# Optimization experiments

Hardware: AMD Instinct MI355X
Metric: run time of the kernel (lower is better)

## Reference

```python
import jax, jax.numpy as jnp
import numpy as np

OUT = 7          # roi_align output size
SR = 2           # sampling_ratio
SCALE = 1.0 / 16.0
T_OUT = 16       # F.interpolate temporal target
EPS = 1e-6


def setup_inputs() -> dict:
    key = jax.random.key(0)
    ks = jax.random.split(key, 12)
    B, Cin, Cout, T, H, W = 1, 1536, 3072, 16, 14, 14
    y = jax.random.normal(ks[0], (B, Cin, T, H, W), jnp.float32)
    x_t = jax.random.normal(ks[1], (B, Cout, T, H, W), jnp.float32)
    # ROIs in 224x224 image coords (spatial_scale = 1/16): one [1,4] box per frame
    x1 = jax.random.uniform(ks[2], (T,), minval=0.0, maxval=112.0)
    y1 = jax.random.uniform(ks[3], (T,), minval=0.0, maxval=112.0)
    x2 = jnp.minimum(x1 + jax.random.uniform(ks[4], (T,), minval=80.0, maxval=112.0), 224.0)
    y2 = jnp.minimum(y1 + jax.random.uniform(ks[5], (T,), minval=80.0, maxval=112.0), 224.0)
    rois = jnp.stack([x1, y1, x2, y2], axis=-1)[:, None, :]  # [T,1,4]
    conv_w = jax.random.normal(ks[6], (Cout, Cin), jnp.float32) * 0.02
    conv_b = jax.random.normal(ks[7], (Cout,), jnp.float32) * 0.02
    gamma = 1.0 + 0.1 * jax.random.normal(ks[8], (Cout,), jnp.float32)
    beta = 0.1 * jax.random.normal(ks[9], (Cout,), jnp.float32)
    run_mean = 0.1 * jax.random.normal(ks[10], (Cout,), jnp.float32)
    run_var = jax.random.uniform(ks[11], (Cout,), minval=0.5, maxval=1.5)
    return dict(y=y, x_t=x_t, rois=rois, conv_w=conv_w, conv_b=conv_b,
                gamma=gamma, beta=beta, run_mean=run_mean, run_var=run_var)


def _bilinear_sample(img, ys, xs):
    # img: [C,H,W]; ys: [Sy]; xs: [Sx] -> [C,Sy,Sx]; torchvision roi_align semantics
    C, H, W = img.shape
    oy = (ys < -1.0) | (ys > H)
    ox = (xs < -1.0) | (xs > W)
    yc = jnp.clip(ys, 0.0, H - 1)
    xc = jnp.clip(xs, 0.0, W - 1)
    y0 = jnp.floor(yc).astype(jnp.int32)
    x0 = jnp.floor(xc).astype(jnp.int32)
    y1i = jnp.minimum(y0 + 1, H - 1)
    x1i = jnp.minimum(x0 + 1, W - 1)
    ly = yc - y0
    lx = xc - x0
    g = lambda yi, xi: img[:, yi[:, None], xi[None, :]]  # [C,Sy,Sx]
    wy0, wy1 = (1.0 - ly)[:, None], ly[:, None]
    wx0, wx1 = (1.0 - lx)[None, :], lx[None, :]
    val = (wy0 * wx0 * g(y0, x0) + wy0 * wx1 * g(y0, x1i)
           + wy1 * wx0 * g(y1i, x0) + wy1 * wx1 * g(y1i, x1i))
    mask = (~oy)[:, None] & (~ox)[None, :]
    return jnp.where(mask[None], val, 0.0)


def _roi_align(feat, boxes):
    # feat: [N,C,H,W]; boxes: [N,4] (one box per image, aligned=False, sampling_ratio=2)
    N, C, H, W = feat.shape
    b = boxes * SCALE
    bx1, by1, bx2, by2 = b[:, 0], b[:, 1], b[:, 2], b[:, 3]
    rw = jnp.maximum(bx2 - bx1, 1.0)
    rh = jnp.maximum(by2 - by1, 1.0)
    bw, bh = rw / OUT, rh / OUT
    # sample positions per bin: (bin + (i+0.5)/SR) * bin_size
    pos = (jnp.arange(OUT, dtype=jnp.float32)[:, None]
           + (jnp.arange(SR, dtype=jnp.float32)[None, :] + 0.5) / SR).reshape(-1)  # [OUT*SR]
    ys = by1[:, None] + pos[None, :] * bh[:, None]
    xs = bx1[:, None] + pos[None, :] * bw[:, None]
    vals = jax.vmap(_bilinear_sample)(feat, ys, xs)  # [N,C,OUT*SR,OUT*SR]
    return vals.reshape(N, C, OUT, SR, OUT, SR).mean(axis=(3, 5))


def reference(y, x_t, rois, conv_w, conv_b, gamma, beta, run_mean, run_var):
    B, Cout, T, Hf, Wf = x_t.shape
    # 1x1x1 Conv3d, stride (1,2,2)
    ys = y[:, :, :, ::2, ::2]                                   # [B,Cin,T,7,7]
    yp = jnp.einsum('bcthw,oc->bothw', ys, conv_w) + conv_b[None, :, None, None, None]
    # BatchNorm3d (eval, eps=1e-6) + GELU (exact)
    inv = gamma / jnp.sqrt(run_var + EPS)
    yp = (yp - run_mean[None, :, None, None, None]) * inv[None, :, None, None, None] \
         + beta[None, :, None, None, None]
    yp = jax.nn.gelu(yp, approximate=False)
    # nearest temporal interpolation to T_OUT (identity when Tin == 16)
    Tin = yp.shape[2]
    tidx = (jnp.arange(T_OUT) * Tin) // T_OUT
    yp = yp[:, :, tidx]                                          # [B,Cout,16,7,7]
    # fusion branch: roi_align over (B*T) frames
    ff = jnp.transpose(x_t, (0, 2, 1, 3, 4)).reshape(B * T, Cout, Hf, Wf)
    boxes = rois[:, 0, :]                                        # [T,4]
    mr = _roi_align(ff, boxes)                                   # [B*T,Cout,7,7]
    mr = jnp.transpose(mr.reshape(B, T, Cout, OUT, OUT), (0, 2, 1, 3, 4))
    weighted = yp * mr                                           # [B,Cout,16,7,7]
    # per-frame 7x7 scatter-write into zeros, same window logic as the torch loop
    bs = boxes * SCALE
    sxi = jnp.floor(bs[:, 0]).astype(jnp.int32)
    syi = jnp.floor(bs[:, 1]).astype(jnp.int32)
    exi = jnp.ceil(bs[:, 2]).astype(jnp.int32)
    eyi = jnp.ceil(bs[:, 3]).astype(jnp.int32)
    ml = jnp.where(sxi + 7 < 14, sxi, exi - 7)
    mt = jnp.where(syi + 7 < 14, syi, eyi - 7)
    def place(w_t, t_off, l_off):  # w_t: [B,Cout,7,7]
        z = jnp.zeros((B, Cout, Hf, Wf), w_t.dtype)
        return jax.lax.dynamic_update_slice(z, w_t, (0, 0, t_off, l_off))
    new_face = jax.vmap(place, in_axes=(2, 0, 0), out_axes=2)(weighted, mt, ml)
    return new_face + x_t
```

## Files before the change

kernel.cpp:

```cpp
#include <hip/hip_runtime.h>

#define KD 1536
#define ND 3072
#define MD 784
#define TT 16

typedef __attribute__((ext_vector_type(8))) short short8;
typedef __attribute__((ext_vector_type(4))) float floatx4;

__device__ __forceinline__ unsigned short f2bf(float f) {
    unsigned int x = __float_as_uint(f);
    unsigned int r = (x + 0x7fffu + ((x >> 16) & 1u)) >> 16;
    return (unsigned short)r;
}

__device__ __forceinline__ void gld_lds16(const unsigned short* g, unsigned short* l) {
    __builtin_amdgcn_global_load_lds((const __attribute__((address_space(1))) void*)g,
                                     (__attribute__((address_space(3))) void*)l, 16, 0, 0);
}

__global__ __launch_bounds__(256) void prep_k(const float* __restrict__ y,
                                              const float* __restrict__ conv_w,
                                              unsigned short* __restrict__ Ap,
                                              unsigned short* __restrict__ Bp) {
    __shared__ float sm[64 * 197];
    const int bid = blockIdx.x;
    const int tid = threadIdx.x;

    if (bid < 384) {
        const int t2 = bid / 24, kc = bid % 24;
        for (int i4 = tid; i4 < 64 * 49; i4 += 256) {
            int c = i4 / 49, p4 = i4 % 49;
            float4 v = *(const float4*)(y + (size_t)(kc * 64 + c) * 3136 + t2 * 196 + p4 * 4);
            float* d = &sm[c * 197 + p4 * 4];
            d[0] = v.x; d[1] = v.y; d[2] = v.z; d[3] = v.w;
        }
        __syncthreads();
        for (int item = tid; item < 64 * 49; item += 256) {
            int c = item & 63, ij = item >> 6;
            int i = ij / 7, j = ij % 7;
            Ap[(size_t)(t2 * 49 + ij) * KD + kc * 64 + c] =
                f2bf(sm[c * 197 + (2 * i) * 14 + 2 * j]);
        }
    } else {
        size_t base = (size_t)(bid - 384) * 12288;
#pragma unroll
        for (int v = 0; v < 12; ++v) {
            size_t e = base + v * 1024 + tid * 4;
            float4 w4 = *(const float4*)(conv_w + e);
            ushort4 o;
            o.x = f2bf(w4.x); o.y = f2bf(w4.y); o.z = f2bf(w4.z); o.w = f2bf(w4.w);
            *(ushort4*)(Bp + e) = o;
        }
    }
}

__global__ __launch_bounds__(256, 3) void gemm_k(const unsigned short* __restrict__ Ap,
                                                 const unsigned short* __restrict__ Bp,
                                                 const float* __restrict__ cb,
                                                 const float* __restrict__ gm,
                                                 const float* __restrict__ bt,
                                                 const float* __restrict__ rm,
                                                 const float* __restrict__ rv,
                                                 const float* __restrict__ x_t,
                                                 const float* __restrict__ rois,
                                                 float* __restrict__ out) {
    __shared__ float sm[64 * 197];
    __shared__ float wx0s[14], wx1s[14], wy0s[14], wy1s[14];
    __shared__ int x0s[14], x1s[14], y0s[14], y1s[14], vxs[14], vys[14];

    unsigned short* const smem = (unsigned short*)sm;
    unsigned short* const As0 = smem;
    unsigned short* const As1 = smem + 4096;
    unsigned short* const Bs0 = smem + 8192;
    unsigned short* const Bs1 = smem + 12288;

    const int tid = threadIdx.x;
    const int n0 = blockIdx.x * 64;
    const int t = blockIdx.y;
    const int aRow0 = t * 49;
    const int wv = tid >> 6;
    const int lane = tid & 63;
    const int wm = wv >> 1, wn = wv & 1;
    const int l15 = lane & 15, quad = lane >> 4;
    const int prow = lane >> 3, pch = lane & 7;
    const int L = pch ^ (prow & 7);

    if (tid < 14) {
        float b0 = rois[t * 4 + 0] * 0.0625f, b1 = rois[t * 4 + 1] * 0.0625f;
        float b2 = rois[t * 4 + 2] * 0.0625f, b3 = rois[t * 4 + 3] * 0.0625f;
        float rw = fmaxf(b2 - b0, 1.0f), rh = fmaxf(b3 - b1, 1.0f);
        float bw = rw * (1.0f / 7.0f), bh = rh * (1.0f / 7.0f);
        int p = tid;
        float pos = (float)(p >> 1) + 0.25f + 0.5f * (float)(p & 1);
        float xs = b0 + pos * bw;
        float ysv = b1 + pos * bh;
        vxs[p] = (xs >= -1.0f && xs <= 14.0f);
        vys[p] = (ysv >= -1.0f && ysv <= 14.0f);
        float xc = fminf(fmaxf(xs, 0.0f), 13.0f);
        float yc = fminf(fmaxf(ysv, 0.0f), 13.0f);
        int x0 = (int)floorf(xc), y0 = (int)floorf(yc);
        x0s[p] = x0; y0s[p] = y0;
        x1s[p] = min(x0 + 1, 13); y1s[p] = min(y0 + 1, 13);
        float lx = xc - (float)x0, ly = yc - (float)y0;
        wx0s[p] = 1.0f - lx; wx1s[p] = lx; wy0s[p] = 1.0f - ly; wy1s[p] = ly;
    }

    const unsigned short* gbase;
    unsigned short *lb0, *lb1;
    if (wv < 2) {
        gbase = Ap + (size_t)(aRow0 + wv * 32 + prow) * KD + L * 8;
        lb0 = &As0[(wv * 32) * 64];
        lb1 = &As1[(wv * 32) * 64];
    } else {
        gbase = Bp + (size_t)(n0 + (wv - 2) * 32 + prow) * KD + L * 8;
        lb0 = &Bs0[((wv - 2) * 32) * 64];
        lb1 = &Bs1[((wv - 2) * 32) * 64];
    }

    floatx4 acc[2][2];
    acc[0][0] = floatx4{0.f, 0.f, 0.f, 0.f};
    acc[0][1] = floatx4{0.f, 0.f, 0.f, 0.f};
    acc[1][0] = floatx4{0.f, 0.f, 0.f, 0.f};
    acc[1][1] = floatx4{0.f, 0.f, 0.f, 0.f};

#pragma unroll
    for (int j = 0; j < 4; ++j)
        gld_lds16(gbase + (size_t)j * 8 * KD, lb0 + j * 512);

    int p = 0;
    for (int kt = 0; kt < KD; kt += 64, p ^= 1) {
        __syncthreads();
        if (kt + 64 < KD) {
            unsigned short* lb = p ? lb0 : lb1;
            const unsigned short* gb = gbase + kt + 64;
#pragma unroll
            for (int j = 0; j < 4; ++j)
                gld_lds16(gb + (size_t)j * 8 * KD, lb + j * 512);
        }
        const unsigned short* Ab = p ? As1 : As0;
        const unsigned short* Bb = p ? Bs1 : Bs0;
#pragma unroll
        for (int ko = 0; ko < 2; ++ko) {
            int ch = ((ko * 4 + quad) ^ (l15 & 7)) * 8;
            short8 a0 = *(const short8*)(Ab + (wm * 32 + l15) * 64 + ch);
            short8 a1 = *(const short8*)(Ab + (wm * 32 + 16 + l15) * 64 + ch);
            short8 b0 = *(const short8*)(Bb + (wn * 32 + l15) * 64 + ch);
            short8 b1 = *(const short8*)(Bb + (wn * 32 + 16 + l15) * 64 + ch);
            acc[0][0] = __builtin_amdgcn_mfma_f32_16x16x32_bf16(a0, b0, acc[0][0], 0, 0, 0);
            acc[0][1] = __builtin_amdgcn_mfma_f32_16x16x32_bf16(a0, b1, acc[0][1], 0, 0, 0);
            acc[1][0] = __builtin_amdgcn_mfma_f32_16x16x32_bf16(a1, b0, acc[1][0], 0, 0, 0);
            acc[1][1] = __builtin_amdgcn_mfma_f32_16x16x32_bf16(a1, b1, acc[1][1], 0, 0, 0);
        }
    }

    __syncthreads();
    for (int i4 = tid; i4 < 64 * 49; i4 += 256) {
        int c = i4 / 49, p4 = i4 % 49;
        float4 xv = *(const float4*)(x_t + (size_t)(n0 + c) * 3136 + t * 196 + p4 * 4);
        float* d = &sm[c * 197 + p4 * 4];
        d[0] = xv.x; d[1] = xv.y; d[2] = xv.z; d[3] = xv.w;
    }
    __syncthreads();

#pragma unroll
    for (int ni = 0; ni < 2; ++ni) {
        const int cl = wn * 32 + ni * 16 + l15;
        const int n = n0 + cl;
        const float scale = gm[n] / sqrtf(rv[n] + 1e-6f);
        const float shift = (cb[n] - rm[n]) * scale + bt[n];
        const float* base = &sm[cl * 197];
#pragma unroll
        for (int mi = 0; mi < 2; ++mi) {
#pragma unroll
            for (int r = 0; r < 4; ++r) {
                const int m = wm * 32 + mi * 16 + quad * 4 + r;
                if (m < 49) {
                    const int i = m / 7, j = m % 7;
                    float sum = 0.0f;
#pragma unroll
                    for (int s = 0; s < 2; ++s) {
                        int pp = 2 * i + s;
#pragma unroll
                        for (int u = 0; u < 2; ++u) {
                            int q = 2 * j + u;
                            if (vys[pp] && vxs[q]) {
                                float v00 = base[y0s[pp] * 14 + x0s[q]];
                                float v01 = base[y0s[pp] * 14 + x1s[q]];
                                float v10 = base[y1s[pp] * 14 + x0s[q]];
                                float v11 = base[y1s[pp] * 14 + x1s[q]];
                                sum += wy0s[pp] * (wx0s[q] * v00 + wx1s[q] * v01) +
                                       wy1s[pp] * (wx0s[q] * v10 + wx1s[q] * v11);
                            }
                        }
                    }
                    const float mrv = 0.25f * sum;
                    const float v = acc[mi][ni][r] * scale + shift;
                    const float g = 0.5f * v * (1.0f + erff(v * 0.70710678118654752f));
                    acc[mi][ni][r] = g * mrv;
                }
            }
        }
    }
    __syncthreads();

    float b0 = rois[t * 4 + 0] * 0.0625f, b1 = rois[t * 4 + 1] * 0.0625f;
    float b2 = rois[t * 4 + 2] * 0.0625f, b3 = rois[t * 4 + 3] * 0.0625f;
    int sxi = (int)floorf(b0), syi = (int)floorf(b1);
    int exi = (int)ceilf(b2), eyi = (int)ceilf(b3);
    int ml = (sxi + 7 < 14) ? sxi : exi - 7;
    int mt = (syi + 7 < 14) ? syi : eyi - 7;
    ml = min(max(ml, 0), 7);
    mt = min(max(mt, 0), 7);

#pragma unroll
    for (int ni = 0; ni < 2; ++ni) {
        const int cl = wn * 32 + ni * 16 + l15;
#pragma unroll
        for (int mi = 0; mi < 2; ++mi) {
#pragma unroll
            for (int r = 0; r < 4; ++r) {
                const int m = wm * 32 + mi * 16 + quad * 4 + r;
                if (m < 49) {
                    const int i = m / 7, j = m % 7;
                    sm[cl * 197 + (mt + i) * 14 + (ml + j)] += acc[mi][ni][r];
                }
            }
        }
    }
    __syncthreads();

    for (int i4 = tid; i4 < 64 * 49; i4 += 256) {
        int c = i4 / 49, p4 = i4 % 49;
        const float* d = &sm[c * 197 + p4 * 4];
        size_t e0 = (size_t)(n0 + c) * 3136 + t * 196 + p4 * 4;
        *(float4*)(out + e0) = make_float4(d[0], d[1], d[2], d[3]);
    }
}

extern "C" void kernel_launch(void* const* d_in, const int* in_sizes, int n_in,
                              void* d_out, int out_size, void* d_ws, size_t ws_size,
                              hipStream_t stream) {
    const float* y = (const float*)d_in[0];
    const float* x_t = (const float*)d_in[1];
    const float* rois = (const float*)d_in[2];
    const float* conv_w = (const float*)d_in[3];
    const float* cb = (const float*)d_in[4];
    const float* gm = (const float*)d_in[5];
    const float* bt = (const float*)d_in[6];
    const float* rm = (const float*)d_in[7];
    const float* rv = (const float*)d_in[8];
    float* out = (float*)d_out;

    char* ws = (char*)d_ws;
    unsigned short* Ap = (unsigned short*)ws;
    unsigned short* Bp = (unsigned short*)(ws + 2555904);

    prep_k<<<768, 256, 0, stream>>>(y, conv_w, Ap, Bp);
    gemm_k<<<dim3(ND / 64, TT), 256, 0, stream>>>(Ap, Bp, cb, gm, bt, rm, rv, x_t, rois, out);
}
```

Before: 165.4 us.

## Triple-buffer GEMM LDS staging with explicit vmcnt waits

Replaces the double-buffered global-to-LDS pipeline with a three-stage ring that issues loads two k-tiles ahead. A manual s_waitcnt vmcnt and a raw s_barrier replace __syncthreads, so loads for later tiles can stay in flight while the current tile is consumed. The aim is to hide more global-load latency in the K loop. It adds LDS usage (six 8KB buffers, which fit inside the existing 64x197 float array) and depends on exact vmcnt accounting for correctness.

```diff
diff --git a/kernel.cpp b/kernel.cpp
--- a/kernel.cpp
+++ b/kernel.cpp
@@ -4,6 +4,7 @@
 #define ND 3072
 #define MD 784
 #define TT 16
+#define NT (KD / 64)
 
 typedef __attribute__((ext_vector_type(8))) short short8;
 typedef __attribute__((ext_vector_type(4))) float floatx4;
@@ -70,10 +71,6 @@
     __shared__ int x0s[14], x1s[14], y0s[14], y1s[14], vxs[14], vys[14];
 
     unsigned short* const smem = (unsigned short*)sm;
-    unsigned short* const As0 = smem;
-    unsigned short* const As1 = smem + 4096;
-    unsigned short* const Bs0 = smem + 8192;
-    unsigned short* const Bs1 = smem + 12288;
 
     const int tid = threadIdx.x;
     const int n0 = blockIdx.x * 64;
@@ -106,17 +103,26 @@
         wx0s[p] = 1.0f - lx; wx1s[p] = lx; wy0s[p] = 1.0f - ly; wy1s[p] = ly;
     }
 
+    unsigned short *A0 = smem,          *A1 = smem + 4096,  *A2 = smem + 8192;
+    unsigned short *B0 = smem + 12288,  *B1 = smem + 16384, *B2 = smem + 20480;
+
     const unsigned short* gbase;
-    unsigned short *lb0, *lb1;
+    int dstoff;
     if (wv < 2) {
         gbase = Ap + (size_t)(aRow0 + wv * 32 + prow) * KD + L * 8;
-        lb0 = &As0[(wv * 32) * 64];
-        lb1 = &As1[(wv * 32) * 64];
+        dstoff = (wv * 32) * 64;
     } else {
         gbase = Bp + (size_t)(n0 + (wv - 2) * 32 + prow) * KD + L * 8;
-        lb0 = &Bs0[((wv - 2) * 32) * 64];
-        lb1 = &Bs1[((wv - 2) * 32) * 64];
-    }
+        dstoff = ((wv - 2) * 32) * 64;
+    }
+
+    auto stage = [&](unsigned short* aT, unsigned short* bT, int kt) {
+        unsigned short* dst = (wv < 2 ? aT : bT) + dstoff;
+        const unsigned short* gb = gbase + kt;
+#pragma unroll
+        for (int j = 0; j < 4; ++j)
+            gld_lds16(gb + (size_t)j * 8 * KD, dst + j * 512);
+    };
 
     floatx4 acc[2][2];
     acc[0][0] = floatx4{0.f, 0.f, 0.f, 0.f};
@@ -124,22 +130,21 @@
     acc[1][0] = floatx4{0.f, 0.f, 0.f, 0.f};
     acc[1][1] = floatx4{0.f, 0.f, 0.f, 0.f};
 
-#pragma unroll
-    for (int j = 0; j < 4; ++j)
-        gld_lds16(gbase + (size_t)j * 8 * KD, lb0 + j * 512);
-
-    int p = 0;
-    for (int kt = 0; kt < KD; kt += 64, p ^= 1) {
-        __syncthreads();
-        if (kt + 64 < KD) {
-            unsigned short* lb = p ? lb0 : lb1;
-            const unsigned short* gb = gbase + kt + 64;
-#pragma unroll
-            for (int j = 0; j < 4; ++j)
-                gld_lds16(gb + (size_t)j * 8 * KD, lb + j * 512);
-        }
-        const unsigned short* Ab = p ? As1 : As0;
-        const unsigned short* Bb = p ? Bs1 : Bs0;
+    stage(A0, B0, 0);
+    stage(A1, B1, 64);
+
+    for (int i = 0; i < NT; ++i) {
+        if (i < NT - 1)
+            asm volatile("s_waitcnt vmcnt(4)" ::: "memory");
+        else
+            asm volatile("s_waitcnt vmcnt(0)" ::: "memory");
+        __builtin_amdgcn_s_barrier();
+        __builtin_amdgcn_sched_barrier(0);
+        if (i + 2 < NT)
+            stage(A2, B2, (i + 2) * 64);
+
+        const unsigned short* Ab = A0;
+        const unsigned short* Bb = B0;
 #pragma unroll
         for (int ko = 0; ko < 2; ++ko) {
             int ch = ((ko * 4 + quad) ^ (l15 & 7)) * 8;
@@ -152,6 +157,9 @@
             acc[1][0] = __builtin_amdgcn_mfma_f32_16x16x32_bf16(a1, b0, acc[1][0], 0, 0, 0);
             acc[1][1] = __builtin_amdgcn_mfma_f32_16x16x32_bf16(a1, b1, acc[1][1], 0, 0, 0);
         }
+
+        unsigned short* tA = A0; A0 = A1; A1 = A2; A2 = tA;
+        unsigned short* tB = B0; B0 = B1; B1 = B2; B2 = tB;
     }
 
     __syncthreads();
```

Result: no change. 167.4 us (+1.2%).

## Shrink GEMM tile to 64x32 with two-wave blocks and vectorized LDS staging

Applied to the files above, without the earlier changes.

The fused GEMM+epilogue kernel now uses 128-thread blocks covering 32 output channels instead of 64. This doubles the grid to 96x16 blocks for better occupancy and load balance. Each wave stages both A and B tiles itself and computes a 32x32 sub-tile. LDS rows are padded to 196/204 floats so x_t staging and output writeback use float4 LDS accesses. The roi validity branches are folded into zeroed interpolation weights, which removes divergent conditionals, at the cost of loading the A tile twice as often per output.

```diff
diff --git a/kernel.cpp b/kernel.cpp
--- a/kernel.cpp
+++ b/kernel.cpp
@@ -23,7 +23,7 @@
                                               const float* __restrict__ conv_w,
                                               unsigned short* __restrict__ Ap,
                                               unsigned short* __restrict__ Bp) {
-    __shared__ float sm[64 * 197];
+    __shared__ __align__(16) float sm[64 * 204];
     const int bid = blockIdx.x;
     const int tid = threadIdx.x;
 
@@ -32,15 +32,14 @@
         for (int i4 = tid; i4 < 64 * 49; i4 += 256) {
             int c = i4 / 49, p4 = i4 % 49;
             float4 v = *(const float4*)(y + (size_t)(kc * 64 + c) * 3136 + t2 * 196 + p4 * 4);
-            float* d = &sm[c * 197 + p4 * 4];
-            d[0] = v.x; d[1] = v.y; d[2] = v.z; d[3] = v.w;
+            *(float4*)(&sm[c * 204 + p4 * 4]) = v;
         }
         __syncthreads();
         for (int item = tid; item < 64 * 49; item += 256) {
             int c = item & 63, ij = item >> 6;
             int i = ij / 7, j = ij % 7;
             Ap[(size_t)(t2 * 49 + ij) * KD + kc * 64 + c] =
-                f2bf(sm[c * 197 + (2 * i) * 14 + 2 * j]);
+                f2bf(sm[c * 204 + (2 * i) * 14 + 2 * j]);
         }
     } else {
         size_t base = (size_t)(bid - 384) * 12288;
@@ -55,7 +54,7 @@
     }
 }
 
-__global__ __launch_bounds__(256, 3) void gemm_k(const unsigned short* __restrict__ Ap,
+__global__ __launch_bounds__(128, 3) void gemm_k(const unsigned short* __restrict__ Ap,
                                                  const unsigned short* __restrict__ Bp,
                                                  const float* __restrict__ cb,
                                                  const float* __restrict__ gm,
@@ -65,26 +64,25 @@
                                                  const float* __restrict__ x_t,
                                                  const float* __restrict__ rois,
                                                  float* __restrict__ out) {
-    __shared__ float sm[64 * 197];
+    __shared__ __align__(16) float sm[32 * 196];
     __shared__ float wx0s[14], wx1s[14], wy0s[14], wy1s[14];
-    __shared__ int x0s[14], x1s[14], y0s[14], y1s[14], vxs[14], vys[14];
+    __shared__ int x0s[14], x1s[14], y0s[14], y1s[14];
 
     unsigned short* const smem = (unsigned short*)sm;
     unsigned short* const As0 = smem;
     unsigned short* const As1 = smem + 4096;
     unsigned short* const Bs0 = smem + 8192;
-    unsigned short* const Bs1 = smem + 12288;
+    unsigned short* const Bs1 = smem + 10240;
 
     const int tid = threadIdx.x;
-    const int n0 = blockIdx.x * 64;
+    const int n0 = blockIdx.x * 32;
     const int t = blockIdx.y;
     const int aRow0 = t * 49;
     const int wv = tid >> 6;
     const int lane = tid & 63;
-    const int wm = wv >> 1, wn = wv & 1;
     const int l15 = lane & 15, quad = lane >> 4;
     const int prow = lane >> 3, pch = lane & 7;
-    const int L = pch ^ (prow & 7);
+    const int L = pch ^ prow;
 
     if (tid < 14) {
         float b0 = rois[t * 4 + 0] * 0.0625f, b1 = rois[t * 4 + 1] * 0.0625f;
@@ -95,28 +93,29 @@
         float pos = (float)(p >> 1) + 0.25f + 0.5f * (float)(p & 1);
         float xs = b0 + pos * bw;
         float ysv = b1 + pos * bh;
-        vxs[p] = (xs >= -1.0f && xs <= 14.0f);
-        vys[p] = (ysv >= -1.0f && ysv <= 14.0f);
+        bool vx = (xs >= -1.0f && xs <= 14.0f);
+        bool vy = (ysv >= -1.0f && ysv <= 14.0f);
         float xc = fminf(fmaxf(xs, 0.0f), 13.0f);
         float yc = fminf(fmaxf(ysv, 0.0f), 13.0f);
         int x0 = (int)floorf(xc), y0 = (int)floorf(yc);
         x0s[p] = x0; y0s[p] = y0;
         x1s[p] = min(x0 + 1, 13); y1s[p] = min(y0 + 1, 13);
         float lx = xc - (float)x0, ly = yc - (float)y0;
-        wx0s[p] = 1.0f - lx; wx1s[p] = lx; wy0s[p] = 1.0f - ly; wy1s[p] = ly;
-    }
-
-    const unsigned short* gbase;
-    unsigned short *lb0, *lb1;
-    if (wv < 2) {
-        gbase = Ap + (size_t)(aRow0 + wv * 32 + prow) * KD + L * 8;
-        lb0 = &As0[(wv * 32) * 64];
-        lb1 = &As1[(wv * 32) * 64];
-    } else {
-        gbase = Bp + (size_t)(n0 + (wv - 2) * 32 + prow) * KD + L * 8;
-        lb0 = &Bs0[((wv - 2) * 32) * 64];
-        lb1 = &Bs1[((wv - 2) * 32) * 64];
-    }
+        wx0s[p] = vx ? (1.0f - lx) : 0.0f; wx1s[p] = vx ? lx : 0.0f;
+        wy0s[p] = vy ? (1.0f - ly) : 0.0f; wy1s[p] = vy ? ly : 0.0f;
+    }
+
+    const unsigned short* gA = Ap + (size_t)(aRow0 + wv * 32 + prow) * KD + L * 8;
+    const unsigned short* gB = Bp + (size_t)(n0 + wv * 16 + prow) * KD + L * 8;
+
+    auto stage = [&](unsigned short* aB, unsigned short* bB, int kt) {
+#pragma unroll
+        for (int v = 0; v < 4; ++v)
+            gld_lds16(gA + (size_t)v * 8 * KD + kt, aB + wv * 2048 + v * 512);
+#pragma unroll
+        for (int v = 0; v < 2; ++v)
+            gld_lds16(gB + (size_t)v * 8 * KD + kt, bB + wv * 1024 + v * 512);
+    };
 
     floatx4 acc[2][2];
     acc[0][0] = floatx4{0.f, 0.f, 0.f, 0.f};
@@ -124,29 +123,21 @@
     acc[1][0] = floatx4{0.f, 0.f, 0.f, 0.f};
     acc[1][1] = floatx4{0.f, 0.f, 0.f, 0.f};
 
-#pragma unroll
-    for (int j = 0; j < 4; ++j)
-        gld_lds16(gbase + (size_t)j * 8 * KD, lb0 + j * 512);
-
+    stage(As0, Bs0, 0);
     int p = 0;
     for (int kt = 0; kt < KD; kt += 64, p ^= 1) {
         __syncthreads();
-        if (kt + 64 < KD) {
-            unsigned short* lb = p ? lb0 : lb1;
-            const unsigned short* gb = gbase + kt + 64;
-#pragma unroll
-            for (int j = 0; j < 4; ++j)
-                gld_lds16(gb + (size_t)j * 8 * KD, lb + j * 512);
-        }
+        if (kt + 64 < KD)
+            stage(p ? As0 : As1, p ? Bs0 : Bs1, kt + 64);
         const unsigned short* Ab = p ? As1 : As0;
         const unsigned short* Bb = p ? Bs1 : Bs0;
 #pragma unroll
         for (int ko = 0; ko < 2; ++ko) {
             int ch = ((ko * 4 + quad) ^ (l15 & 7)) * 8;
-            short8 a0 = *(const short8*)(Ab + (wm * 32 + l15) * 64 + ch);
-            short8 a1 = *(const short8*)(Ab + (wm * 32 + 16 + l15) * 64 + ch);
-            short8 b0 = *(const short8*)(Bb + (wn * 32 + l15) * 64 + ch);
-            short8 b1 = *(const short8*)(Bb + (wn * 32 + 16 + l15) * 64 + ch);
+            short8 a0 = *(const short8*)(Ab + (wv * 32 + l15) * 64 + ch);
+            short8 a1 = *(const short8*)(Ab + (wv * 32 + 16 + l15) * 64 + ch);
+            short8 b0 = *(const short8*)(Bb + (l15) * 64 + ch);
+            short8 b1 = *(const short8*)(Bb + (16 + l15) * 64 + ch);
             acc[0][0] = __builtin_amdgcn_mfma_f32_16x16x32_bf16(a0, b0, acc[0][0], 0, 0, 0);
             acc[0][1] = __builtin_amdgcn_mfma_f32_16x16x32_bf16(a0, b1, acc[0][1], 0, 0, 0);
             acc[1][0] = __builtin_amdgcn_mfma_f32_16x16x32_bf16(a1, b0, acc[1][0], 0, 0, 0);
@@ -155,26 +146,25 @@
     }
 
     __syncthreads();
-    for (int i4 = tid; i4 < 64 * 49; i4 += 256) {
+    for (int i4 = tid; i4 < 32 * 49; i4 += 128) {
         int c = i4 / 49, p4 = i4 % 49;
         float4 xv = *(const float4*)(x_t + (size_t)(n0 + c) * 3136 + t * 196 + p4 * 4);
-        float* d = &sm[c * 197 + p4 * 4];
-        d[0] = xv.x; d[1] = xv.y; d[2] = xv.z; d[3] = xv.w;
+        *(float4*)(&sm[c * 196 + p4 * 4]) = xv;
     }
     __syncthreads();
 
 #pragma unroll
     for (int ni = 0; ni < 2; ++ni) {
-        const int cl = wn * 32 + ni * 16 + l15;
+        const int cl = ni * 16 + l15;
         const int n = n0 + cl;
         const float scale = gm[n] / sqrtf(rv[n] + 1e-6f);
         const float shift = (cb[n] - rm[n]) * scale + bt[n];
-        const float* base = &sm[cl * 197];
+        const float* base = &sm[cl * 196];
 #pragma unroll
         for (int mi = 0; mi < 2; ++mi) {
 #pragma unroll
             for (int r = 0; r < 4; ++r) {
-                const int m = wm * 32 + mi * 16 + quad * 4 + r;
+                const int m = wv * 32 + mi * 16 + quad * 4 + r;
                 if (m < 49) {
                     const int i = m / 7, j = m % 7;
                     float sum = 0.0f;
@@ -184,14 +174,12 @@
 #pragma unroll
                         for (int u = 0; u < 2; ++u) {
                             int q = 2 * j + u;
-                            if (vys[pp] && vxs[q]) {
-                                float v00 = base[y0s[pp] * 14 + x0s[q]];
-                                float v01 = base[y0s[pp] * 14 + x1s[q]];
-                                float v10 = base[y1s[pp] * 14 + x0s[q]];
-                                float v11 = base[y1s[pp] * 14 + x1s[q]];
-                                sum += wy0s[pp] * (wx0s[q] * v00 + wx1s[q] * v01) +
-                                       wy1s[pp] * (wx0s[q] * v10 + wx1s[q] * v11);
-                            }
+                            float v00 = base[y0s[pp] * 14 + x0s[q]];
+                            float v01 = base[y0s[pp] * 14 + x1s[q]];
+                            float v10 = base[y1s[pp] * 14 + x0s[q]];
+                            float v11 = base[y1s[pp] * 14 + x1s[q]];
+                            sum += wy0s[pp] * (wx0s[q] * v00 + wx1s[q] * v01) +
+                                   wy1s[pp] * (wx0s[q] * v10 + wx1s[q] * v11);
                         }
                     }
                     const float mrv = 0.25f * sum;
@@ -215,26 +203,26 @@
 
 #pragma unroll
     for (int ni = 0; ni < 2; ++ni) {
-        const int cl = wn * 32 + ni * 16 + l15;
+        const int cl = ni * 16 + l15;
 #pragma unroll
         for (int mi = 0; mi < 2; ++mi) {
 #pragma unroll
             for (int r = 0; r < 4; ++r) {
-                const int m = wm * 32 + mi * 16 + quad * 4 + r;
+                const int m = wv * 32 + mi * 16 + quad * 4 + r;
                 if (m < 49) {
                     const int i = m / 7, j = m % 7;
-                    sm[cl * 197 + (mt + i) * 14 + (ml + j)] += acc[mi][ni][r];
+                    sm[cl * 196 + (mt + i) * 14 + (ml + j)] += acc[mi][ni][r];
                 }
             }
         }
     }
     __syncthreads();
 
-    for (int i4 = tid; i4 < 64 * 49; i4 += 256) {
+    for (int i4 = tid; i4 < 32 * 49; i4 += 128) {
         int c = i4 / 49, p4 = i4 % 49;
-        const float* d = &sm[c * 197 + p4 * 4];
+        float4 xv = *(const float4*)(&sm[c * 196 + p4 * 4]);
         size_t e0 = (size_t)(n0 + c) * 3136 + t * 196 + p4 * 4;
-        *(float4*)(out + e0) = make_float4(d[0], d[1], d[2], d[3]);
+        *(float4*)(out + e0) = xv;
     }
 }
 
@@ -257,5 +245,5 @@
     unsigned short* Bp = (unsigned short*)(ws + 2555904);
 
     prep_k<<<768, 256, 0, stream>>>(y, conv_w, Ap, Bp);
-    gemm_k<<<dim3(ND / 64, TT), 256, 0, stream>>>(Ap, Bp, cb, gm, bt, rm, rv, x_t, rois, out);
-}
+    gemm_k<<<dim3(ND / 32, TT), 128, 0, stream>>>(Ap, Bp, cb, gm, bt, rm, rv, x_t, rois, out);
+}
```

Measured after the change: 161.3 us. 1.03x faster.
